# Performance work log

Hardware: AMD Instinct MI355X
Metric: run time of the kernel (lower is better)

Reference implementation:

```python
import jax, jax.numpy as jnp
import numpy as np

B, T, D, H = 4096, 1024, 3, 64


def setup_inputs() -> dict:
    key = jax.random.key(0)
    ks = jax.random.split(key, 10)
    s_ih = 1.0 / np.sqrt(H)
    return {
        "x1": jax.random.normal(ks[0], (B, T, D), dtype=jnp.float32),
        "x2": jax.random.normal(ks[1], (B, T, D), dtype=jnp.float32),
        # PyTorch nn.GRU params, gate order (r, z, n)
        "W_ih": jax.random.uniform(ks[2], (3 * H, D), jnp.float32, -s_ih, s_ih),
        "W_hh": jax.random.uniform(ks[3], (3 * H, H), jnp.float32, -s_ih, s_ih),
        "b_ih": jax.random.uniform(ks[4], (3 * H,), jnp.float32, -s_ih, s_ih),
        "b_hh": jax.random.uniform(ks[5], (3 * H,), jnp.float32, -s_ih, s_ih),
        # MLP head: Linear(64,32) -> ReLU -> Linear(32,1) -> Sigmoid
        "W1": jax.random.uniform(ks[6], (32, H), jnp.float32, -s_ih, s_ih),
        "b1": jax.random.uniform(ks[7], (32,), jnp.float32, -s_ih, s_ih),
        "W2": jax.random.uniform(ks[8], (1, 32), jnp.float32, -1 / np.sqrt(32), 1 / np.sqrt(32)),
        "b2": jax.random.uniform(ks[9], (1,), jnp.float32, -1 / np.sqrt(32), 1 / np.sqrt(32)),
    }


def _gru_last_hidden(x, W_ih, W_hh, b_ih, b_hh):
    # x: [B, T, D] -> final hidden state [B, H], PyTorch GRU semantics.
    xs = jnp.swapaxes(x, 0, 1)  # [T, B, D]

    def step(h, xt):
        xg = xt @ W_ih.T + b_ih            # [B, 3H]
        hg = h @ W_hh.T + b_hh             # [B, 3H]
        xr, xz, xn = jnp.split(xg, 3, axis=-1)
        hr, hz, hn = jnp.split(hg, 3, axis=-1)
        r = jax.nn.sigmoid(xr + hr)
        z = jax.nn.sigmoid(xz + hz)
        n = jnp.tanh(xn + r * hn)
        h_new = (1.0 - z) * n + z * h
        return h_new, None

    h0 = jnp.zeros((x.shape[0], W_hh.shape[1]), dtype=x.dtype)
    h_last, _ = jax.lax.scan(step, h0, xs)
    return h_last


def reference(x1, x2, W_ih, W_hh, b_ih, b_hh, W1, b1, W2, b2):
    h1 = _gru_last_hidden(x1, W_ih, W_hh, b_ih, b_hh)
    h2 = _gru_last_hidden(x2, W_ih, W_hh, b_ih, b_hh)
    diff = jnp.abs(h1 - h2)                                # [B, H]
    hid = jax.nn.relu(diff @ W1.T + b1)                    # [B, 32]
    out = jax.nn.sigmoid(hid @ W2.T + b2)                  # [B, 1]
    return out
```

## Files before the change

### kernel.cpp

```cpp
#include <hip/hip_runtime.h>
#include <math.h>

#define T_ 1024
#define D_ 3
#define H_ 64

typedef _Float16 f16x8 __attribute__((ext_vector_type(8)));
typedef float f32x4 __attribute__((ext_vector_type(4)));

__device__ __forceinline__ float sigmoid_f(float x) {
    return __builtin_amdgcn_rcpf(1.0f + __expf(-x));
}

#define MFMA(A, B, C) __builtin_amdgcn_mfma_f32_16x16x32_f16((A), (B), (C), 0, 0, 0)

__global__ __launch_bounds__(256, 2) void gru_mfma5(
    const float* __restrict__ x1, const float* __restrict__ x2,
    const float* __restrict__ W_ih, const float* __restrict__ W_hh,
    const float* __restrict__ b_ih, const float* __restrict__ b_hh,
    const float* __restrict__ W1, const float* __restrict__ b1,
    const float* __restrict__ W2, const float* __restrict__ b2,
    float* __restrict__ out)
{
    const int lane = threadIdx.x & 63;
    const int w    = threadIdx.x >> 6;
    const int c    = lane & 15;
    const int q    = lane >> 4;
    const int u    = 16 * w + c;
    const int seq0 = blockIdx.x * 8;

    const float SRZ = -1.44269504f;
    const float SN  =  2.88539008f;
    const float gsc[3] = {SRZ, SRZ, SN};

    f16x8 wf[3][2];
    #pragma unroll
    for (int g = 0; g < 3; ++g)
        #pragma unroll
        for (int ks = 0; ks < 2; ++ks) {
            const float* p = W_hh + (size_t)(g * 64 + u) * H_ + 32 * ks + q * 8;
            f16x8 v;
            #pragma unroll
            for (int j = 0; j < 8; ++j) v[j] = (_Float16)(p[j] * gsc[g]);
            wf[g][ks] = v;
        }

    f16x8 bxf[3];
    #pragma unroll
    for (int g = 0; g < 3; ++g) {
        f16x8 v = {};
        if (q == 0) {
            #pragma unroll
            for (int d = 0; d < 3; ++d)
                v[d] = (_Float16)(W_ih[(size_t)(g * 64 + u) * D_ + d] * gsc[g]);
        }
        bxf[g] = v;
    }

    const float comb_r = (b_ih[u]      + b_hh[u])      * SRZ;
    const float comb_z = (b_ih[64 + u] + b_hh[64 + u]) * SRZ;
    const float bxn    = b_ih[128 + u] * SN;
    const float bhn    = b_hh[128 + u] * SN;
    const f32x4 Cr  = {comb_r, comb_r, comb_r, comb_r};
    const f32x4 Cz  = {comb_z, comb_z, comb_z, comb_z};
    const f32x4 Cxn = {bxn, bxn, bxn, bxn};
    const f32x4 Chn = {bhn, bhn, bhn, bhn};

    const float* xptr = (c < 8) ? (x1 + (size_t)(seq0 + c) * (T_ * D_))
                                : (x2 + (size_t)(seq0 + c - 8) * (T_ * D_));

    __shared__ alignas(16) _Float16 hb[2][16 * 72];
    __shared__ float dlds[8][68];

    float h[4];
    #pragma unroll
    for (int r = 0; r < 4; ++r) h[r] = 0.f;

    auto step = [&](int buf, float x0, float x1v, float x2v) {
        #pragma unroll
        for (int r = 0; r < 4; ++r)
            hb[buf][(4 * q + r) * 72 + u] = (_Float16)h[r];
        f16x8 ax = {};
        ax[0] = (_Float16)x0; ax[1] = (_Float16)x1v; ax[2] = (_Float16)x2v;
        f32x4 ar  = MFMA(ax, bxf[0], Cr);
        f32x4 az  = MFMA(ax, bxf[1], Cz);
        f32x4 axn = MFMA(ax, bxf[2], Cxn);
        __syncthreads();
        const f16x8 a0 = *(const f16x8*)&hb[buf][c * 72 + q * 8];
        const f16x8 a1 = *(const f16x8*)&hb[buf][c * 72 + 32 + q * 8];

        ar  = MFMA(a0, wf[0][0], ar);
        az  = MFMA(a0, wf[1][0], az);
        f32x4 ahn = MFMA(a0, wf[2][0], Chn);
        ar  = MFMA(a1, wf[0][1], ar);
        az  = MFMA(a1, wf[1][1], az);
        ahn = MFMA(a1, wf[2][1], ahn);

        #pragma unroll
        for (int r = 0; r < 4; ++r) {
            const float eu = __builtin_amdgcn_exp2f(ar[r]);
            const float ev = __builtin_amdgcn_exp2f(az[r]);
            const float pu = 1.0f + eu, pv = 1.0f + ev;
            const float inv = __builtin_amdgcn_rcpf(pu * pv);
            const float rr = pv * inv;
            const float zz = pu * inv;
            const float tt = axn[r] + rr * ahn[r];
            const float e2 = __builtin_amdgcn_exp2f(tt);
            const float nn = 1.0f - 2.0f * __builtin_amdgcn_rcpf(e2 + 1.0f);
            h[r] = nn + zz * (h[r] - nn);
        }
    };

    const float4* xp4 = (const float4*)xptr;
    float4 xc[3];
    #pragma unroll
    for (int i = 0; i < 3; ++i) xc[i] = xp4[i];

    for (int t = 0; t < T_; t += 4) {
        float4 xn[3];
        const int tb = (t + 4 < T_) ? (3 * (t + 4)) / 4 : (3 * t) / 4;
        #pragma unroll
        for (int i = 0; i < 3; ++i) xn[i] = xp4[tb + i];
        step(0, xc[0].x, xc[0].y, xc[0].z);
        step(1, xc[0].w, xc[1].x, xc[1].y);
        step(0, xc[1].z, xc[1].w, xc[2].x);
        step(1, xc[2].y, xc[2].z, xc[2].w);
        #pragma unroll
        for (int i = 0; i < 3; ++i) xc[i] = xn[i];
    }

    #pragma unroll
    for (int r = 0; r < 4; ++r) {
        const float o = __shfl_xor(h[r], 32);
        if (q < 2) dlds[4 * q + r][u] = fabsf(h[r] - o);
    }
    __syncthreads();
    if (w == 0) {
        const int s = lane >> 3;
        const int b = lane & 7;
        float am[4];
        #pragma unroll
        for (int i = 0; i < 4; ++i) am[i] = b1[b + 8 * i];
        #pragma unroll
        for (int k4 = 0; k4 < 16; ++k4) {
            const float4 dvec = *(const float4*)&dlds[s][k4 * 4];
            #pragma unroll
            for (int i = 0; i < 4; ++i) {
                const float4 wv = *(const float4*)&W1[(b + 8 * i) * H_ + k4 * 4];
                am[i] += dvec.x * wv.x + dvec.y * wv.y + dvec.z * wv.z + dvec.w * wv.w;
            }
        }
        float part = 0.f;
        #pragma unroll
        for (int i = 0; i < 4; ++i) part += fmaxf(am[i], 0.f) * W2[b + 8 * i];
        part += __shfl_xor(part, 1);
        part += __shfl_xor(part, 2);
        part += __shfl_xor(part, 4);
        if (b == 0) out[seq0 + s] = sigmoid_f(part + b2[0]);
    }
}

extern "C" void kernel_launch(void* const* d_in, const int* in_sizes, int n_in,
                              void* d_out, int out_size, void* d_ws, size_t ws_size,
                              hipStream_t stream) {
    const float* x1   = (const float*)d_in[0];
    const float* x2   = (const float*)d_in[1];
    const float* W_ih = (const float*)d_in[2];
    const float* W_hh = (const float*)d_in[3];
    const float* b_ih = (const float*)d_in[4];
    const float* b_hh = (const float*)d_in[5];
    const float* W1   = (const float*)d_in[6];
    const float* b1   = (const float*)d_in[7];
    const float* W2   = (const float*)d_in[8];
    const float* b2   = (const float*)d_in[9];

    const int B = in_sizes[0] / (T_ * D_);
    dim3 grid(B / 8), block(256);
    gru_mfma5<<<grid, block, 0, stream>>>(x1, x2, W_ih, W_hh, b_ih, b_hh,
                                          W1, b1, W2, b2, (float*)d_out);
}
```

Before: 579.8 us.

## Process two independent 8-sequence groups per block to interleave recurrences

Each block now runs two independent GRU recurrences (16 sequence pairs) together, sharing one barrier per timestep and interleaving their MFMA and transcendental chains. This amortizes the per-step __syncthreads and gives the scheduler independent work to hide MFMA and exp latency. In exchange it halves the grid to 256 blocks, relaxes launch bounds to one block per SIMD group, and doubles register and LDS use per block.

```diff
diff --git a/kernel.cpp b/kernel.cpp
--- a/kernel.cpp
+++ b/kernel.cpp
@@ -14,7 +14,7 @@
 
 #define MFMA(A, B, C) __builtin_amdgcn_mfma_f32_16x16x32_f16((A), (B), (C), 0, 0, 0)
 
-__global__ __launch_bounds__(256, 2) void gru_mfma5(
+__global__ __launch_bounds__(256, 1) void gru_mfma6(
     const float* __restrict__ x1, const float* __restrict__ x2,
     const float* __restrict__ W_ih, const float* __restrict__ W_hh,
     const float* __restrict__ b_ih, const float* __restrict__ b_hh,
@@ -27,7 +27,8 @@
     const int c    = lane & 15;
     const int q    = lane >> 4;
     const int u    = 16 * w + c;
-    const int seq0 = blockIdx.x * 8;
+    const int seqA = blockIdx.x * 16;
+    const int seqB = seqA + 8;
 
     const float SRZ = -1.44269504f;
     const float SN  =  2.88539008f;
@@ -66,84 +67,123 @@
     const f32x4 Cxn = {bxn, bxn, bxn, bxn};
     const f32x4 Chn = {bhn, bhn, bhn, bhn};
 
-    const float* xptr = (c < 8) ? (x1 + (size_t)(seq0 + c) * (T_ * D_))
-                                : (x2 + (size_t)(seq0 + c - 8) * (T_ * D_));
-
-    __shared__ alignas(16) _Float16 hb[2][16 * 72];
-    __shared__ float dlds[8][68];
-
-    float h[4];
-    #pragma unroll
-    for (int r = 0; r < 4; ++r) h[r] = 0.f;
-
-    auto step = [&](int buf, float x0, float x1v, float x2v) {
-        #pragma unroll
-        for (int r = 0; r < 4; ++r)
-            hb[buf][(4 * q + r) * 72 + u] = (_Float16)h[r];
-        f16x8 ax = {};
-        ax[0] = (_Float16)x0; ax[1] = (_Float16)x1v; ax[2] = (_Float16)x2v;
-        f32x4 ar  = MFMA(ax, bxf[0], Cr);
-        f32x4 az  = MFMA(ax, bxf[1], Cz);
-        f32x4 axn = MFMA(ax, bxf[2], Cxn);
+    const float* xpA = (c < 8) ? (x1 + (size_t)(seqA + c) * (T_ * D_))
+                               : (x2 + (size_t)(seqA + c - 8) * (T_ * D_));
+    const float* xpB = (c < 8) ? (x1 + (size_t)(seqB + c) * (T_ * D_))
+                               : (x2 + (size_t)(seqB + c - 8) * (T_ * D_));
+
+    __shared__ alignas(16) _Float16 hbA[2][16 * 72];
+    __shared__ alignas(16) _Float16 hbB[2][16 * 72];
+    __shared__ float dlds[16][68];
+
+    float hA[4], hB[4];
+    #pragma unroll
+    for (int r = 0; r < 4; ++r) { hA[r] = 0.f; hB[r] = 0.f; }
+
+    auto step = [&](int buf, float a0, float a1v, float a2v,
+                             float b0, float b1v, float b2v) {
+        #pragma unroll
+        for (int r = 0; r < 4; ++r) {
+            hbA[buf][(4 * q + r) * 72 + u] = (_Float16)hA[r];
+            hbB[buf][(4 * q + r) * 72 + u] = (_Float16)hB[r];
+        }
+        f16x8 axA = {};
+        axA[0] = (_Float16)a0; axA[1] = (_Float16)a1v; axA[2] = (_Float16)a2v;
+        f16x8 axB = {};
+        axB[0] = (_Float16)b0; axB[1] = (_Float16)b1v; axB[2] = (_Float16)b2v;
+        f32x4 arA  = MFMA(axA, bxf[0], Cr);
+        f32x4 azA  = MFMA(axA, bxf[1], Cz);
+        f32x4 axnA = MFMA(axA, bxf[2], Cxn);
+        f32x4 arB  = MFMA(axB, bxf[0], Cr);
+        f32x4 azB  = MFMA(axB, bxf[1], Cz);
+        f32x4 axnB = MFMA(axB, bxf[2], Cxn);
         __syncthreads();
-        const f16x8 a0 = *(const f16x8*)&hb[buf][c * 72 + q * 8];
-        const f16x8 a1 = *(const f16x8*)&hb[buf][c * 72 + 32 + q * 8];
-
-        ar  = MFMA(a0, wf[0][0], ar);
-        az  = MFMA(a0, wf[1][0], az);
-        f32x4 ahn = MFMA(a0, wf[2][0], Chn);
-        ar  = MFMA(a1, wf[0][1], ar);
-        az  = MFMA(a1, wf[1][1], az);
-        ahn = MFMA(a1, wf[2][1], ahn);
+        const f16x8 aA0 = *(const f16x8*)&hbA[buf][c * 72 + q * 8];
+        const f16x8 aA1 = *(const f16x8*)&hbA[buf][c * 72 + 32 + q * 8];
+        const f16x8 aB0 = *(const f16x8*)&hbB[buf][c * 72 + q * 8];
+        const f16x8 aB1 = *(const f16x8*)&hbB[buf][c * 72 + 32 + q * 8];
+
+        arA  = MFMA(aA0, wf[0][0], arA);
+        azA  = MFMA(aA0, wf[1][0], azA);
+        f32x4 ahnA = MFMA(aA0, wf[2][0], Chn);
+        arA  = MFMA(aA1, wf[0][1], arA);
+        azA  = MFMA(aA1, wf[1][1], azA);
+        ahnA = MFMA(aA1, wf[2][1], ahnA);
+
+        arB  = MFMA(aB0, wf[0][0], arB);
+        azB  = MFMA(aB0, wf[1][0], azB);
+        f32x4 ahnB = MFMA(aB0, wf[2][0], Chn);
+        arB  = MFMA(aB1, wf[0][1], arB);
+        azB  = MFMA(aB1, wf[1][1], azB);
+        ahnB = MFMA(aB1, wf[2][1], ahnB);
 
         #pragma unroll
         for (int r = 0; r < 4; ++r) {
-            const float eu = __builtin_amdgcn_exp2f(ar[r]);
-            const float ev = __builtin_amdgcn_exp2f(az[r]);
+            const float eu = __builtin_amdgcn_exp2f(arA[r]);
+            const float ev = __builtin_amdgcn_exp2f(azA[r]);
             const float pu = 1.0f + eu, pv = 1.0f + ev;
             const float inv = __builtin_amdgcn_rcpf(pu * pv);
             const float rr = pv * inv;
             const float zz = pu * inv;
-            const float tt = axn[r] + rr * ahn[r];
+            const float tt = axnA[r] + rr * ahnA[r];
             const float e2 = __builtin_amdgcn_exp2f(tt);
             const float nn = 1.0f - 2.0f * __builtin_amdgcn_rcpf(e2 + 1.0f);
-            h[r] = nn + zz * (h[r] - nn);
+            hA[r] = nn + zz * (hA[r] - nn);
+        }
+        #pragma unroll
+        for (int r = 0; r < 4; ++r) {
+            const float eu = __builtin_amdgcn_exp2f(arB[r]);
+            const float ev = __builtin_amdgcn_exp2f(azB[r]);
+            const float pu = 1.0f + eu, pv = 1.0f + ev;
+            const float inv = __builtin_amdgcn_rcpf(pu * pv);
+            const float rr = pv * inv;
+            const float zz = pu * inv;
+            const float tt = axnB[r] + rr * ahnB[r];
+            const float e2 = __builtin_amdgcn_exp2f(tt);
+            const float nn = 1.0f - 2.0f * __builtin_amdgcn_rcpf(e2 + 1.0f);
+            hB[r] = nn + zz * (hB[r] - nn);
         }
     };
 
-    const float4* xp4 = (const float4*)xptr;
-    float4 xc[3];
-    #pragma unroll
-    for (int i = 0; i < 3; ++i) xc[i] = xp4[i];
+    const float4* x4A = (const float4*)xpA;
+    const float4* x4B = (const float4*)xpB;
+    float4 cA[3], cB[3];
+    #pragma unroll
+    for (int i = 0; i < 3; ++i) { cA[i] = x4A[i]; cB[i] = x4B[i]; }
 
     for (int t = 0; t < T_; t += 4) {
-        float4 xn[3];
+        float4 nA[3], nB[3];
         const int tb = (t + 4 < T_) ? (3 * (t + 4)) / 4 : (3 * t) / 4;
         #pragma unroll
-        for (int i = 0; i < 3; ++i) xn[i] = xp4[tb + i];
-        step(0, xc[0].x, xc[0].y, xc[0].z);
-        step(1, xc[0].w, xc[1].x, xc[1].y);
-        step(0, xc[1].z, xc[1].w, xc[2].x);
-        step(1, xc[2].y, xc[2].z, xc[2].w);
-        #pragma unroll
-        for (int i = 0; i < 3; ++i) xc[i] = xn[i];
+        for (int i = 0; i < 3; ++i) { nA[i] = x4A[tb + i]; nB[i] = x4B[tb + i]; }
+        step(0, cA[0].x, cA[0].y, cA[0].z,  cB[0].x, cB[0].y, cB[0].z);
+        step(1, cA[0].w, cA[1].x, cA[1].y,  cB[0].w, cB[1].x, cB[1].y);
+        step(0, cA[1].z, cA[1].w, cA[2].x,  cB[1].z, cB[1].w, cB[2].x);
+        step(1, cA[2].y, cA[2].z, cA[2].w,  cB[2].y, cB[2].z, cB[2].w);
+        #pragma unroll
+        for (int i = 0; i < 3; ++i) { cA[i] = nA[i]; cB[i] = nB[i]; }
     }
 
     #pragma unroll
     for (int r = 0; r < 4; ++r) {
-        const float o = __shfl_xor(h[r], 32);
-        if (q < 2) dlds[4 * q + r][u] = fabsf(h[r] - o);
+        const float oA = __shfl_xor(hA[r], 32);
+        const float oB = __shfl_xor(hB[r], 32);
+        if (q < 2) {
+            dlds[4 * q + r][u]     = fabsf(hA[r] - oA);
+            dlds[8 + 4 * q + r][u] = fabsf(hB[r] - oB);
+        }
     }
     __syncthreads();
-    if (w == 0) {
+    if (w < 2) {
         const int s = lane >> 3;
         const int b = lane & 7;
+        const float* dl = &dlds[8 * w + s][0];
         float am[4];
         #pragma unroll
         for (int i = 0; i < 4; ++i) am[i] = b1[b + 8 * i];
         #pragma unroll
         for (int k4 = 0; k4 < 16; ++k4) {
-            const float4 dvec = *(const float4*)&dlds[s][k4 * 4];
+            const float4 dvec = *(const float4*)&dl[k4 * 4];
             #pragma unroll
             for (int i = 0; i < 4; ++i) {
                 const float4 wv = *(const float4*)&W1[(b + 8 * i) * H_ + k4 * 4];
@@ -156,7 +196,7 @@
         part += __shfl_xor(part, 1);
         part += __shfl_xor(part, 2);
         part += __shfl_xor(part, 4);
-        if (b == 0) out[seq0 + s] = sigmoid_f(part + b2[0]);
+        if (b == 0) out[(w == 0 ? seqA : seqB) + s] = sigmoid_f(part + b2[0]);
     }
 }
 
@@ -175,7 +215,7 @@
     const float* b2   = (const float*)d_in[9];
 
     const int B = in_sizes[0] / (T_ * D_);
-    dim3 grid(B / 8), block(256);
-    gru_mfma5<<<grid, block, 0, stream>>>(x1, x2, W_ih, W_hh, b_ih, b_hh,
+    dim3 grid(B / 16), block(256);
+    gru_mfma6<<<grid, block, 0, stream>>>(x1, x2, W_ih, W_hh, b_ih, b_hh,
                                           W1, b1, W2, b2, (float*)d_out);
 }
```

After: 774.0 us. 1.33x slower.

## Ping-pong two sequence groups per block so MFMA and gate math overlap

Applied to the files above, without the earlier changes.

Each block now holds two independent groups of 8 sequences in 512 threads. The groups are phase-shifted so one runs its MFMA phase (A) while the other runs its transcendental gate phase (B). A lightweight s_waitcnt+s_barrier separates the phases. The h write to LDS moves to the end of the gate phase, so each half-step needs only one barrier shared across both groups. The aim is to hide the serial latency of the recurrence by interleaving the matrix and vector units. The cost is barriers that span 8 waves, and the occupancy bound changes from (256,2) to (512,1).

```diff
diff --git a/kernel.cpp b/kernel.cpp
--- a/kernel.cpp
+++ b/kernel.cpp
@@ -13,8 +13,9 @@
 }
 
 #define MFMA(A, B, C) __builtin_amdgcn_mfma_f32_16x16x32_f16((A), (B), (C), 0, 0, 0)
-
-__global__ __launch_bounds__(256, 2) void gru_mfma5(
+#define LBAR() asm volatile("s_waitcnt lgkmcnt(0)\n\ts_barrier" ::: "memory")
+
+__global__ __launch_bounds__(512, 1) void gru_mfma8(
     const float* __restrict__ x1, const float* __restrict__ x2,
     const float* __restrict__ W_ih, const float* __restrict__ W_hh,
     const float* __restrict__ b_ih, const float* __restrict__ b_hh,
@@ -22,12 +23,15 @@
     const float* __restrict__ W2, const float* __restrict__ b2,
     float* __restrict__ out)
 {
-    const int lane = threadIdx.x & 63;
-    const int w    = threadIdx.x >> 6;
+    const int tid  = threadIdx.x;
+    const int lane = tid & 63;
+    const int wv   = tid >> 6;
+    const int g    = wv >> 2;
+    const int w    = wv & 3;
     const int c    = lane & 15;
     const int q    = lane >> 4;
     const int u    = 16 * w + c;
-    const int seq0 = blockIdx.x * 8;
+    const int seq0 = blockIdx.x * 16 + g * 8;
 
     const float SRZ = -1.44269504f;
     const float SN  =  2.88539008f;
@@ -35,26 +39,26 @@
 
     f16x8 wf[3][2];
     #pragma unroll
-    for (int g = 0; g < 3; ++g)
+    for (int gg = 0; gg < 3; ++gg)
         #pragma unroll
         for (int ks = 0; ks < 2; ++ks) {
-            const float* p = W_hh + (size_t)(g * 64 + u) * H_ + 32 * ks + q * 8;
+            const float* p = W_hh + (size_t)(gg * 64 + u) * H_ + 32 * ks + q * 8;
             f16x8 v;
             #pragma unroll
-            for (int j = 0; j < 8; ++j) v[j] = (_Float16)(p[j] * gsc[g]);
-            wf[g][ks] = v;
+            for (int j = 0; j < 8; ++j) v[j] = (_Float16)(p[j] * gsc[gg]);
+            wf[gg][ks] = v;
         }
 
     f16x8 bxf[3];
     #pragma unroll
-    for (int g = 0; g < 3; ++g) {
+    for (int gg = 0; gg < 3; ++gg) {
         f16x8 v = {};
         if (q == 0) {
             #pragma unroll
             for (int d = 0; d < 3; ++d)
-                v[d] = (_Float16)(W_ih[(size_t)(g * 64 + u) * D_ + d] * gsc[g]);
-        }
-        bxf[g] = v;
+                v[d] = (_Float16)(W_ih[(size_t)(gg * 64 + u) * D_ + d] * gsc[gg]);
+        }
+        bxf[gg] = v;
     }
 
     const float comb_r = (b_ih[u]      + b_hh[u])      * SRZ;
@@ -69,33 +73,31 @@
     const float* xptr = (c < 8) ? (x1 + (size_t)(seq0 + c) * (T_ * D_))
                                 : (x2 + (size_t)(seq0 + c - 8) * (T_ * D_));
 
-    __shared__ alignas(16) _Float16 hb[2][16 * 72];
-    __shared__ float dlds[8][68];
+    __shared__ alignas(16) _Float16 hb[2][2][16 * 72];
+    __shared__ float dlds[2][8][68];
 
     float h[4];
     #pragma unroll
     for (int r = 0; r < 4; ++r) h[r] = 0.f;
 
-    auto step = [&](int buf, float x0, float x1v, float x2v) {
-        #pragma unroll
-        for (int r = 0; r < 4; ++r)
-            hb[buf][(4 * q + r) * 72 + u] = (_Float16)h[r];
+    f32x4 ar = {}, az = {}, axn = {}, ahn = {};
+
+    auto A = [&](int buf, float x0, float x1v, float x2v) {
+        const f16x8 a0 = *(const f16x8*)&hb[g][buf][c * 72 + q * 8];
+        const f16x8 a1 = *(const f16x8*)&hb[g][buf][c * 72 + 32 + q * 8];
         f16x8 ax = {};
         ax[0] = (_Float16)x0; ax[1] = (_Float16)x1v; ax[2] = (_Float16)x2v;
-        f32x4 ar  = MFMA(ax, bxf[0], Cr);
-        f32x4 az  = MFMA(ax, bxf[1], Cz);
-        f32x4 axn = MFMA(ax, bxf[2], Cxn);
-        __syncthreads();
-        const f16x8 a0 = *(const f16x8*)&hb[buf][c * 72 + q * 8];
-        const f16x8 a1 = *(const f16x8*)&hb[buf][c * 72 + 32 + q * 8];
-
+        ar  = MFMA(ax, bxf[0], Cr);
+        az  = MFMA(ax, bxf[1], Cz);
+        axn = MFMA(ax, bxf[2], Cxn);
         ar  = MFMA(a0, wf[0][0], ar);
         az  = MFMA(a0, wf[1][0], az);
-        f32x4 ahn = MFMA(a0, wf[2][0], Chn);
+        ahn = MFMA(a0, wf[2][0], Chn);
         ar  = MFMA(a1, wf[0][1], ar);
         az  = MFMA(a1, wf[1][1], az);
         ahn = MFMA(a1, wf[2][1], ahn);
-
+    };
+    auto B = [&](int wbuf) {
         #pragma unroll
         for (int r = 0; r < 4; ++r) {
             const float eu = __builtin_amdgcn_exp2f(ar[r]);
@@ -109,30 +111,73 @@
             const float nn = 1.0f - 2.0f * __builtin_amdgcn_rcpf(e2 + 1.0f);
             h[r] = nn + zz * (h[r] - nn);
         }
+        #pragma unroll
+        for (int r = 0; r < 4; ++r)
+            hb[g][wbuf][(4 * q + r) * 72 + u] = (_Float16)h[r];
     };
 
+    #pragma unroll
+    for (int r = 0; r < 4; ++r)
+        hb[g][0][(4 * q + r) * 72 + u] = (_Float16)0.f;
     const float4* xp4 = (const float4*)xptr;
     float4 xc[3];
     #pragma unroll
     for (int i = 0; i < 3; ++i) xc[i] = xp4[i];
-
-    for (int t = 0; t < T_; t += 4) {
+    LBAR();
+    if (g == 0) A(0, xc[0].x, xc[0].y, xc[0].z);
+
+    int t = 0;
+    for (; t < T_ - 4; t += 4) {
         float4 xn[3];
-        const int tb = (t + 4 < T_) ? (3 * (t + 4)) / 4 : (3 * t) / 4;
+        const int tb = (3 * (t + 4)) / 4;
         #pragma unroll
         for (int i = 0; i < 3; ++i) xn[i] = xp4[tb + i];
-        step(0, xc[0].x, xc[0].y, xc[0].z);
-        step(1, xc[0].w, xc[1].x, xc[1].y);
-        step(0, xc[1].z, xc[1].w, xc[2].x);
-        step(1, xc[2].y, xc[2].z, xc[2].w);
+        if (g == 0) {
+            B(1);                                   LBAR();
+            A(1, xc[0].w, xc[1].x, xc[1].y);        LBAR();
+            B(0);                                   LBAR();
+            A(0, xc[1].z, xc[1].w, xc[2].x);        LBAR();
+            B(1);                                   LBAR();
+            A(1, xc[2].y, xc[2].z, xc[2].w);        LBAR();
+            B(0);                                   LBAR();
+            A(0, xn[0].x, xn[0].y, xn[0].z);        LBAR();
+        } else {
+            A(0, xc[0].x, xc[0].y, xc[0].z);        LBAR();
+            B(1);                                   LBAR();
+            A(1, xc[0].w, xc[1].x, xc[1].y);        LBAR();
+            B(0);                                   LBAR();
+            A(0, xc[1].z, xc[1].w, xc[2].x);        LBAR();
+            B(1);                                   LBAR();
+            A(1, xc[2].y, xc[2].z, xc[2].w);        LBAR();
+            B(0);                                   LBAR();
+        }
         #pragma unroll
         for (int i = 0; i < 3; ++i) xc[i] = xn[i];
+    }
+    if (g == 0) {
+        B(1);                                   LBAR();
+        A(1, xc[0].w, xc[1].x, xc[1].y);        LBAR();
+        B(0);                                   LBAR();
+        A(0, xc[1].z, xc[1].w, xc[2].x);        LBAR();
+        B(1);                                   LBAR();
+        A(1, xc[2].y, xc[2].z, xc[2].w);        LBAR();
+        B(0);                                   LBAR();
+        LBAR();
+    } else {
+        A(0, xc[0].x, xc[0].y, xc[0].z);        LBAR();
+        B(1);                                   LBAR();
+        A(1, xc[0].w, xc[1].x, xc[1].y);        LBAR();
+        B(0);                                   LBAR();
+        A(0, xc[1].z, xc[1].w, xc[2].x);        LBAR();
+        B(1);                                   LBAR();
+        A(1, xc[2].y, xc[2].z, xc[2].w);        LBAR();
+        B(0);                                   LBAR();
     }
 
     #pragma unroll
     for (int r = 0; r < 4; ++r) {
         const float o = __shfl_xor(h[r], 32);
-        if (q < 2) dlds[4 * q + r][u] = fabsf(h[r] - o);
+        if (q < 2) dlds[g][4 * q + r][u] = fabsf(h[r] - o);
     }
     __syncthreads();
     if (w == 0) {
@@ -143,11 +188,11 @@
         for (int i = 0; i < 4; ++i) am[i] = b1[b + 8 * i];
         #pragma unroll
         for (int k4 = 0; k4 < 16; ++k4) {
-            const float4 dvec = *(const float4*)&dlds[s][k4 * 4];
+            const float4 dvec = *(const float4*)&dlds[g][s][k4 * 4];
             #pragma unroll
             for (int i = 0; i < 4; ++i) {
-                const float4 wv = *(const float4*)&W1[(b + 8 * i) * H_ + k4 * 4];
-                am[i] += dvec.x * wv.x + dvec.y * wv.y + dvec.z * wv.z + dvec.w * wv.w;
+                const float4 wv2 = *(const float4*)&W1[(b + 8 * i) * H_ + k4 * 4];
+                am[i] += dvec.x * wv2.x + dvec.y * wv2.y + dvec.z * wv2.z + dvec.w * wv2.w;
             }
         }
         float part = 0.f;
@@ -175,7 +220,7 @@
     const float* b2   = (const float*)d_in[9];
 
     const int B = in_sizes[0] / (T_ * D_);
-    dim3 grid(B / 8), block(256);
-    gru_mfma5<<<grid, block, 0, stream>>>(x1, x2, W_ih, W_hh, b_ih, b_hh,
+    dim3 grid(B / 16), block(512);
+    gru_mfma8<<<grid, block, 0, stream>>>(x1, x2, W_ih, W_hh, b_ih, b_hh,
                                           W1, b1, W2, b2, (float*)d_out);
 }
```

Result: slower. 839.4 us (+44.8%).

## Software-pipeline GRU input projection one step ahead and lighten the per-step barrier

Applied to the files above, without the earlier changes.

The input-projection MFMAs for step t+1 are now computed during step t and passed through ping-pong accumulator arrays, so the recurrent MFMA chain starts directly from precomputed values. This takes them off the latency-critical serial path of each step. The __syncthreads is replaced by an inline-asm lgkmcnt wait plus s_barrier, and the MFMA region is wrapped in s_setprio. The LDS row stride changes from 72 to 76 to alter bank mapping, and x loads are double-buffered over an 8-step unroll. In exchange it uses more registers, relies on hand-written barrier asm, and computes one extra projection at the end.

```diff
diff --git a/kernel.cpp b/kernel.cpp
--- a/kernel.cpp
+++ b/kernel.cpp
@@ -4,6 +4,7 @@
 #define T_ 1024
 #define D_ 3
 #define H_ 64
+#define LDH 76
 
 typedef _Float16 f16x8 __attribute__((ext_vector_type(8)));
 typedef float f32x4 __attribute__((ext_vector_type(4)));
@@ -13,8 +14,9 @@
 }
 
 #define MFMA(A, B, C) __builtin_amdgcn_mfma_f32_16x16x32_f16((A), (B), (C), 0, 0, 0)
-
-__global__ __launch_bounds__(256, 2) void gru_mfma5(
+#define LBAR() asm volatile("s_waitcnt lgkmcnt(0)\n\ts_barrier" ::: "memory")
+
+__global__ __launch_bounds__(256, 2) void gru_mfma9(
     const float* __restrict__ x1, const float* __restrict__ x2,
     const float* __restrict__ W_ih, const float* __restrict__ W_hh,
     const float* __restrict__ b_ih, const float* __restrict__ b_hh,
@@ -69,32 +71,35 @@
     const float* xptr = (c < 8) ? (x1 + (size_t)(seq0 + c) * (T_ * D_))
                                 : (x2 + (size_t)(seq0 + c - 8) * (T_ * D_));
 
-    __shared__ alignas(16) _Float16 hb[2][16 * 72];
+    __shared__ alignas(16) _Float16 hb[2][16 * LDH];
     __shared__ float dlds[8][68];
 
     float h[4];
     #pragma unroll
     for (int r = 0; r < 4; ++r) h[r] = 0.f;
 
-    auto step = [&](int buf, float x0, float x1v, float x2v) {
+    auto step = [&](int buf, float nx0, float nx1, float nx2,
+                    f32x4 (&xcur)[3], f32x4 (&xnxt)[3]) {
         #pragma unroll
         for (int r = 0; r < 4; ++r)
-            hb[buf][(4 * q + r) * 72 + u] = (_Float16)h[r];
+            hb[buf][(4 * q + r) * LDH + u] = (_Float16)h[r];
         f16x8 ax = {};
-        ax[0] = (_Float16)x0; ax[1] = (_Float16)x1v; ax[2] = (_Float16)x2v;
-        f32x4 ar  = MFMA(ax, bxf[0], Cr);
-        f32x4 az  = MFMA(ax, bxf[1], Cz);
-        f32x4 axn = MFMA(ax, bxf[2], Cxn);
-        __syncthreads();
-        const f16x8 a0 = *(const f16x8*)&hb[buf][c * 72 + q * 8];
-        const f16x8 a1 = *(const f16x8*)&hb[buf][c * 72 + 32 + q * 8];
-
-        ar  = MFMA(a0, wf[0][0], ar);
-        az  = MFMA(a0, wf[1][0], az);
+        ax[0] = (_Float16)nx0; ax[1] = (_Float16)nx1; ax[2] = (_Float16)nx2;
+        LBAR();
+        __builtin_amdgcn_s_setprio(1);
+        const f16x8 a0 = *(const f16x8*)&hb[buf][c * LDH + q * 8];
+        const f16x8 a1 = *(const f16x8*)&hb[buf][c * LDH + 32 + q * 8];
+        xnxt[0] = MFMA(ax, bxf[0], Cr);
+        xnxt[1] = MFMA(ax, bxf[1], Cz);
+        xnxt[2] = MFMA(ax, bxf[2], Cxn);
+        f32x4 ar  = MFMA(a0, wf[0][0], xcur[0]);
+        f32x4 az  = MFMA(a0, wf[1][0], xcur[1]);
         f32x4 ahn = MFMA(a0, wf[2][0], Chn);
         ar  = MFMA(a1, wf[0][1], ar);
         az  = MFMA(a1, wf[1][1], az);
         ahn = MFMA(a1, wf[2][1], ahn);
+        __builtin_amdgcn_s_setprio(0);
+        const f32x4 axn = xcur[2];
 
         #pragma unroll
         for (int r = 0; r < 4; ++r) {
@@ -112,21 +117,40 @@
     };
 
     const float4* xp4 = (const float4*)xptr;
-    float4 xc[3];
+    float4 xc[3], xd[3];
     #pragma unroll
     for (int i = 0; i < 3; ++i) xc[i] = xp4[i];
-
-    for (int t = 0; t < T_; t += 4) {
-        float4 xn[3];
-        const int tb = (t + 4 < T_) ? (3 * (t + 4)) / 4 : (3 * t) / 4;
-        #pragma unroll
-        for (int i = 0; i < 3; ++i) xn[i] = xp4[tb + i];
-        step(0, xc[0].x, xc[0].y, xc[0].z);
-        step(1, xc[0].w, xc[1].x, xc[1].y);
-        step(0, xc[1].z, xc[1].w, xc[2].x);
-        step(1, xc[2].y, xc[2].z, xc[2].w);
-        #pragma unroll
-        for (int i = 0; i < 3; ++i) xc[i] = xn[i];
+    #pragma unroll
+    for (int i = 0; i < 3; ++i) xd[i] = xp4[3 + i];
+
+    f32x4 xpA[3], xpB[3];
+    {
+        f16x8 ax = {};
+        ax[0] = (_Float16)xc[0].x; ax[1] = (_Float16)xc[0].y; ax[2] = (_Float16)xc[0].z;
+        xpA[0] = MFMA(ax, bxf[0], Cr);
+        xpA[1] = MFMA(ax, bxf[1], Cz);
+        xpA[2] = MFMA(ax, bxf[2], Cxn);
+    }
+
+    for (int t = 0; t < T_; t += 8) {
+        step(0, xc[0].w, xc[1].x, xc[1].y, xpA, xpB);
+        step(1, xc[1].z, xc[1].w, xc[2].x, xpB, xpA);
+        step(0, xc[2].y, xc[2].z, xc[2].w, xpA, xpB);
+        {
+            const int tb = (t + 8 < T_) ? (3 * (t + 8)) / 4 : (3 * t) / 4;
+            #pragma unroll
+            for (int i = 0; i < 3; ++i) xc[i] = xp4[tb + i];
+        }
+        step(1, xd[0].x, xd[0].y, xd[0].z, xpB, xpA);
+        step(0, xd[0].w, xd[1].x, xd[1].y, xpA, xpB);
+        step(1, xd[1].z, xd[1].w, xd[2].x, xpB, xpA);
+        step(0, xd[2].y, xd[2].z, xd[2].w, xpA, xpB);
+        {
+            const int tb = (t + 12 < T_) ? (3 * (t + 12)) / 4 : (3 * t) / 4;
+            #pragma unroll
+            for (int i = 0; i < 3; ++i) xd[i] = xp4[tb + i];
+        }
+        step(1, xc[0].x, xc[0].y, xc[0].z, xpB, xpA);
     }
 
     #pragma unroll
@@ -176,6 +200,6 @@
 
     const int B = in_sizes[0] / (T_ * D_);
     dim3 grid(B / 8), block(256);
-    gru_mfma5<<<grid, block, 0, stream>>>(x1, x2, W_ih, W_hh, b_ih, b_hh,
+    gru_mfma9<<<grid, block, 0, stream>>>(x1, x2, W_ih, W_hh, b_ih, b_hh,
                                           W1, b1, W2, b2, (float*)d_out);
 }
```

Result: slower. 644.2 us (+11.1%).
